# Performance work log

Hardware: AMD Instinct MI355X
Metric: run time of the kernel (lower is better)

Reference implementation:

```python
import jax, jax.numpy as jnp
import numpy as np

SDIM, VDIM, HID, DEPTH = 128, 3, 64, 4
N, E = 50000, 800000
CUTOFF = 5.0


def setup_inputs() -> dict:
    key = jax.random.key(0)
    ks = jax.random.split(key, 16)
    s = jax.random.normal(ks[0], (N, SDIM), jnp.float32)
    v = jax.random.normal(ks[1], (N, 3, VDIM), jnp.float32)
    edge_index = jax.random.randint(ks[2], (2, E), 0, N, dtype=jnp.int32).astype(jnp.int64)
    d = jax.random.uniform(ks[3], (E,), jnp.float32) * CUTOFF
    r = jax.random.normal(ks[4], (E, 3), jnp.float32)
    r = r / jnp.linalg.norm(r, axis=-1, keepdims=True)
    batch = jnp.zeros((N,), jnp.int64)

    def w(k, shape):
        return jax.random.normal(k, shape, jnp.float32) / jnp.sqrt(jnp.float32(shape[-2]))

    return {
        's': s, 'v': v, 'edge_index': edge_index, 'd': d, 'r': r, 'batch': batch,
        'We1': w(ks[5], (DEPTH, 2 * SDIM + 1, HID)), 'be1': jnp.zeros((DEPTH, HID), jnp.float32),
        'We2': w(ks[6], (DEPTH, HID, HID)), 'be2': jnp.zeros((DEPTH, HID), jnp.float32),
        'Wn1': w(ks[7], (DEPTH, SDIM + HID, HID)), 'bn1': jnp.zeros((DEPTH, HID), jnp.float32),
        'Wn2': w(ks[8], (DEPTH, HID, SDIM)), 'bn2': jnp.zeros((DEPTH, SDIM), jnp.float32),
        'Wv': w(ks[9], (DEPTH, HID, 2 * VDIM)), 'bv': jnp.zeros((DEPTH, 2 * VDIM), jnp.float32),
    }


def _egcl(s, v, src, dst, d, r, C, deg, We1, be1, We2, be2, Wn1, bn1, Wn2, bn2, Wv, bv):
    n = s.shape[0]
    # edge message MLP on gathered endpoint features + distance
    x = jnp.concatenate([s[dst], s[src], d[:, None]], axis=-1)   # [E, 2*SDIM+1]
    h = jax.nn.silu(x @ We1 + be1)
    h = jax.nn.silu(h @ We2 + be2)
    h = h * C[:, None]                                            # cutoff envelope
    # scalar update
    agg_s = jax.ops.segment_sum(h, dst, num_segments=n)           # [N, HID]
    u = jax.nn.silu(jnp.concatenate([s, agg_s], axis=-1) @ Wn1 + bn1)
    s = s + (u @ Wn2 + bn2)
    # equivariant vector update: gated neighbor vectors + gated edge directions
    gates = h @ Wv + bv                                           # [E, 2*VDIM]
    g1, g2 = gates[:, :VDIM], gates[:, VDIM:]
    mv = v[src] * g1[:, None, :] + r[:, :, None] * g2[:, None, :] # [E, 3, VDIM]
    agg_v = jax.ops.segment_sum(mv, dst, num_segments=n) / deg[:, None, None]  # mean aggr
    v = v + agg_v
    return s, v


def reference(s, v, edge_index, d, r, batch, We1, be1, We2, be2, Wn1, bn1, Wn2, bn2, Wv, bv):
    src, dst = edge_index[0], edge_index[1]
    C = 0.5 * (jnp.cos(jnp.pi * d / CUTOFF) + 1.0) * (d < CUTOFF).astype(d.dtype)
    deg = jax.ops.segment_sum(jnp.ones_like(d), dst, num_segments=s.shape[0])
    deg = jnp.maximum(deg, 1.0)
    for i in range(DEPTH):
        s, v = _egcl(s, v, src, dst, d, r, C, deg,
                     We1[i], be1[i], We2[i], be2[i],
                     Wn1[i], bn1[i], Wn2[i], bn2[i], Wv[i], bv[i])
    return (s, v)
```

## Files before the change

### kernel.cpp

```cpp
#include <hip/hip_runtime.h>
#include <math.h>

#define SDIM 128
#define HID 64
#define DEPTH 4
#define CUTOFF_F 5.0f
#define CHUNK 4096

typedef __attribute__((ext_vector_type(8))) short bf16x8;
typedef __attribute__((ext_vector_type(4))) float f32x4;
typedef float4 __attribute__((aligned(4))) float4_u;

__device__ __forceinline__ float silu_f(float x) {
    float e = __expf(-x);
    return x * __builtin_amdgcn_rcpf(1.0f + e);
}

__device__ __forceinline__ unsigned short f2bf(float x) {
    unsigned int u = __float_as_uint(x);
    unsigned int r = (u + 0x7fffu + ((u >> 16) & 1u)) >> 16;
    return (unsigned short)r;
}
__device__ __forceinline__ float bf2f(unsigned short u) {
    return __uint_as_float(((unsigned int)u) << 16);
}

struct f8 { float v[8]; };
__device__ __forceinline__ f8 load8(const float* p) {
    f8 r;
    float4 a = *(const float4*)p;
    float4 b = *(const float4*)(p + 4);
    r.v[0]=a.x; r.v[1]=a.y; r.v[2]=a.z; r.v[3]=a.w;
    r.v[4]=b.x; r.v[5]=b.y; r.v[6]=b.z; r.v[7]=b.w;
    return r;
}
__device__ __forceinline__ bf16x8 pack8(const float* h) {
    bf16x8 o;
#pragma unroll
    for (int j = 0; j < 8; ++j) o[j] = (short)f2bf(h[j]);
    return o;
}
__device__ __forceinline__ void unpack8(bf16x8 b, float* o) {
#pragma unroll
    for (int j = 0; j < 8; ++j)
        o[j] = __uint_as_float(((unsigned int)(unsigned short)b[j]) << 16);
}

__global__ void detect_idx_kernel(const void* ei, int N, int* flag) {
    int lane = threadIdx.x;
    const long long* p64 = (const long long*)ei;
    long long v = p64[lane];
    bool ok = (v >= 0 && v < (long long)N);
    unsigned long long m = __ballot(ok);
    if (lane == 0) *flag = (m == ~0ull) ? 1 : 0;
}

__global__ void decode_idx_kernel(const void* ei, int E, int N, const int* flag,
                                  int* __restrict__ srcw, int* __restrict__ dstw,
                                  int* __restrict__ deg_i) {
    int i = blockIdx.x * blockDim.x + threadIdx.x;
    if (i >= 2 * E) return;
    int v;
    if (*flag) v = (int)((const long long*)ei)[i];
    else       v = ((const int*)ei)[i];
    v = min(max(v, 0), N - 1);
    if (i < E) {
        srcw[i] = v;
    } else {
        dstw[i - E] = v;
        atomicAdd(&deg_i[v], 1);
    }
}

__global__ __launch_bounds__(256) void scan1_kernel(const int* __restrict__ deg_i,
                                                    int* __restrict__ part, int N) {
    __shared__ int wsum[4];
    int b = blockIdx.x, t = threadIdx.x;
    int base = b * CHUNK;
    int sum = 0;
    for (int i = t; i < CHUNK; i += 256) {
        int idx = base + i;
        sum += (idx < N) ? deg_i[idx] : 0;
    }
#pragma unroll
    for (int off = 32; off; off >>= 1) sum += __shfl_down(sum, off, 64);
    if ((t & 63) == 0) wsum[t >> 6] = sum;
    __syncthreads();
    if (t == 0) part[b] = wsum[0] + wsum[1] + wsum[2] + wsum[3];
}

__global__ void scan2_kernel(int* __restrict__ part, int* __restrict__ row_start,
                             int B1, int N) {
    int t = threadIdx.x;
    int v = (t < B1) ? part[t] : 0;
    int incl = v;
#pragma unroll
    for (int off = 1; off < 64; off <<= 1) {
        int x = __shfl_up(incl, off, 64);
        if (t >= off) incl += x;
    }
    if (t < B1) part[t] = incl - v;
    if (t == 63) row_start[N] = incl;
}

__global__ __launch_bounds__(256) void scan3_kernel(const int* __restrict__ deg_i,
                                                    const int* __restrict__ part,
                                                    int* __restrict__ row_start, int N) {
    __shared__ int wsum[4];
    __shared__ int carry_s;
    int b = blockIdx.x, t = threadIdx.x;
    int lane = t & 63, w = t >> 6;
    if (t == 0) carry_s = part[b];
    __syncthreads();
    int base0 = b * CHUNK;
    for (int base = base0; base < base0 + CHUNK; base += 256) {
        int i = base + t;
        int v = (i < N) ? deg_i[i] : 0;
        int incl = v;
#pragma unroll
        for (int off = 1; off < 64; off <<= 1) {
            int x = __shfl_up(incl, off, 64);
            if (lane >= off) incl += x;
        }
        if (lane == 63) wsum[w] = incl;
        __syncthreads();
        int wpre = 0;
#pragma unroll
        for (int k = 0; k < 4; ++k) if (k < w) wpre += wsum[k];
        int total = wsum[0] + wsum[1] + wsum[2] + wsum[3];
        int carry = carry_s;
        if (i < N) row_start[i] = carry + wpre + incl - v;
        __syncthreads();
        if (t == 0) carry_s = carry + total;
        __syncthreads();
    }
}

__global__ void scatter_kernel(const int* __restrict__ srcw, const int* __restrict__ dstw,
                               const float* __restrict__ dvec, const float* __restrict__ rvec,
                               const int* __restrict__ row_start, int* __restrict__ cursor,
                               float* __restrict__ rec, int E) {
    int e = blockIdx.x * blockDim.x + threadIdx.x;
    if (e >= E) return;
    int dd = dstw[e];
    int ofs = atomicAdd(&cursor[dd], 1);
    int pos = row_start[dd] + ofs;
    float dv = dvec[e];
    float c = 0.5f * (cosf(3.14159265358979323846f * dv * (1.0f / CUTOFF_F)) + 1.0f);
    c = (dv < CUTOFF_F) ? c : 0.0f;
    float4 r0 = make_float4(__int_as_float(srcw[e]), __int_as_float(dd), dv, c);
    float4 r1 = make_float4(rvec[(size_t)e * 3 + 0], rvec[(size_t)e * 3 + 1],
                            rvec[(size_t)e * 3 + 2], 0.0f);
    *(float4*)(rec + (size_t)pos * 8)     = r0;
    *(float4*)(rec + (size_t)pos * 8 + 4) = r1;
}

__global__ __launch_bounds__(256) void wprep_kernel(
    const float* __restrict__ We1, const float* __restrict__ We2,
    const float* __restrict__ Wv,  const float* __restrict__ Wn1,
    const float* __restrict__ Wn2,
    unsigned short* __restrict__ We1t, unsigned short* __restrict__ We2t,
    unsigned short* __restrict__ Wvt,  unsigned short* __restrict__ Wn1t,
    unsigned short* __restrict__ Wn2t) {
    int l = blockIdx.x, t = threadIdx.x;
    const float* W2 = We2 + (size_t)l * HID * HID;
    unsigned short* T2 = We2t + (size_t)l * HID * HID;
    for (int idx = t; idx < HID * HID; idx += 256) {
        int n = idx >> 6, k = idx & 63;
        T2[n * 64 + k] = f2bf(W2[k * HID + n]);
    }
    const float* Wvl = Wv + (size_t)l * HID * 6;
    unsigned short* Tv = Wvt + (size_t)l * 16 * 64;
    for (int idx = t; idx < 16 * 64; idx += 256) {
        int n = idx >> 6, k = idx & 63;
        Tv[idx] = (n < 6) ? f2bf(Wvl[k * 6 + n]) : (unsigned short)0;
    }
    const float* W1 = We1 + (size_t)l * 257 * 64;
    unsigned short* T1 = We1t + (size_t)l * 128 * 128;
    for (int idx = t; idx < 128 * 128; idx += 256) {
        int n = idx >> 7, k = idx & 127;
        float w = (n < 64) ? W1[(size_t)k * 64 + n] : W1[(size_t)(k + 128) * 64 + (n - 64)];
        T1[n * 128 + k] = f2bf(w);
    }
    const float* Wn1l = Wn1 + (size_t)l * 192 * 64;
    unsigned short* Tn1 = Wn1t + (size_t)l * 64 * 192;
    for (int idx = t; idx < 64 * 192; idx += 256) {
        int n = idx / 192, k = idx - n * 192;
        Tn1[idx] = f2bf(Wn1l[(size_t)k * 64 + n]);
    }
    const float* Wn2l = Wn2 + (size_t)l * 64 * 128;
    unsigned short* Tn2 = Wn2t + (size_t)l * 128 * 64;
    for (int idx = t; idx < 128 * 64; idx += 256) {
        int n = idx >> 6, k = idx & 63;
        Tn2[idx] = f2bf(Wn2l[(size_t)k * 128 + n]);
    }
}

__global__ __launch_bounds__(256) void node_pre_kernel(
    const float* __restrict__ s, const unsigned short* __restrict__ We1t,
    const float* __restrict__ be1,
    unsigned short* __restrict__ Pa, unsigned short* __restrict__ Pb, int N)
{
    __shared__ unsigned short sa[64 * 136];
    int t = threadIdx.x;
    int n0 = blockIdx.x * 64;
    for (int idx = t; idx < 64 * 32; idx += 256) {
        int rn = idx >> 5, c4 = (idx & 31) << 2;
        int n = n0 + rn;
        float4 val = make_float4(0.f, 0.f, 0.f, 0.f);
        if (n < N) val = *(const float4*)(s + (size_t)n * SDIM + c4);
        unsigned int p0 = (unsigned int)f2bf(val.x) | ((unsigned int)f2bf(val.y) << 16);
        unsigned int p1 = (unsigned int)f2bf(val.z) | ((unsigned int)f2bf(val.w) << 16);
        *(uint2*)(sa + rn * 136 + c4) = make_uint2(p0, p1);
    }
    __syncthreads();
    int lane = t & 63, w = t >> 6;
    int lm = lane & 15, lq = lane >> 4;
    int m0 = w * 16, rm = m0 + lm;

    bf16x8 af[4];
#pragma unroll
    for (int kc = 0; kc < 4; ++kc)
        af[kc] = *(const bf16x8*)(sa + rm * 136 + kc * 32 + lq * 8);

#pragma unroll
    for (int ct = 0; ct < 8; ++ct) {
        int col = ct * 16 + lm;
        f32x4 acc = {0.f, 0.f, 0.f, 0.f};
#pragma unroll
        for (int kc = 0; kc < 4; ++kc) {
            bf16x8 b = *(const bf16x8*)(We1t + (size_t)col * 128 + kc * 32 + lq * 8);
            acc = __builtin_amdgcn_mfma_f32_16x16x32_bf16(af[kc], b, acc, 0, 0, 0);
        }
        float bias = (ct < 4) ? be1[col] : 0.0f;
#pragma unroll
        for (int g = 0; g < 4; ++g) {
            int n = n0 + m0 + lq * 4 + g;
            if (n < N) {
                if (ct < 4) Pa[(size_t)n * HID + col]        = f2bf(acc[g] + bias);
                else        Pb[(size_t)n * HID + (col - 64)] = f2bf(acc[g]);
            }
        }
    }
}

__global__ __launch_bounds__(256) void edge_kernel(
    const float* __restrict__ rec,
    const unsigned short* __restrict__ Pa, const unsigned short* __restrict__ Pb,
    const float* __restrict__ wd,
    const unsigned short* __restrict__ We2t, const float* __restrict__ be2,
    const unsigned short* __restrict__ Wvt, const float* __restrict__ bv,
    const float* __restrict__ v,
    float* __restrict__ agg_s, float* __restrict__ agg_v, int E)
{
    __shared__ unsigned short hb[64 * 72];
    __shared__ float gl[64 * 8];
    __shared__ float vb[64 * 12];
    __shared__ int   m_src[64], m_dst[64];
    __shared__ float m_d[64], m_C[64];
    __shared__ float m_r[64 * 3];
    int t = threadIdx.x;
    int e0 = blockIdx.x * 64;
    if (t < 64) {
        int e = e0 + t;
        int ec = (e < E) ? e : (E - 1);
        float4 r0 = *(const float4*)(rec + (size_t)ec * 8);
        float4 r1 = *(const float4*)(rec + (size_t)ec * 8 + 4);
        m_src[t] = __float_as_int(r0.x);
        m_dst[t] = __float_as_int(r0.y);
        m_d[t]   = r0.z;
        m_C[t]   = (e < E) ? r0.w : 0.0f;
        m_r[t*3+0] = r1.x; m_r[t*3+1] = r1.y; m_r[t*3+2] = r1.z;
    }
    __syncthreads();

    int lane = t & 63;
    int w    = t >> 6;
    int lm = lane & 15, lq = lane >> 4;
    int m0 = w * 16;
    int rm = m0 + lm;
    int ka = lq * 8;
    int kb = 32 + lq * 8;

    if (t < 64) {
        const float* vr = v + (size_t)m_src[t] * 9;
        float4_u a = *(const float4_u*)vr;
        float4_u b = *(const float4_u*)(vr + 4);
        float c = vr[8];
        vb[t*12+0]=a.x; vb[t*12+1]=a.y; vb[t*12+2]=a.z; vb[t*12+3]=a.w;
        vb[t*12+4]=b.x; vb[t*12+5]=b.y; vb[t*12+6]=b.z; vb[t*12+7]=b.w;
        vb[t*12+8]=c;
    }
    bf16x8 wv0 = *(const bf16x8*)(Wvt + (size_t)lm * 64 + ka);
    bf16x8 wv1 = *(const bf16x8*)(Wvt + (size_t)lm * 64 + kb);

    bf16x8 afr0, afr1;
    {
        int dstr = m_dst[rm], srcr = m_src[rm];
        float dv = m_d[rm];
        const unsigned short* pa = Pa + (size_t)dstr * HID;
        const unsigned short* pb = Pb + (size_t)srcr * HID;
        bf16x8 ba0 = *(const bf16x8*)(pa + ka);
        bf16x8 bb0 = *(const bf16x8*)(pb + ka);
        bf16x8 ba1 = *(const bf16x8*)(pa + kb);
        bf16x8 bb1 = *(const bf16x8*)(pb + kb);
        f8 xw = load8(wd + ka), yw = load8(wd + kb);
        float fa[8], fb[8], h1[8];
        unpack8(ba0, fa); unpack8(bb0, fb);
#pragma unroll
        for (int j = 0; j < 8; ++j) h1[j] = silu_f(fa[j] + fb[j] + dv * xw.v[j]);
        afr0 = pack8(h1);
        unpack8(ba1, fa); unpack8(bb1, fb);
#pragma unroll
        for (int j = 0; j < 8; ++j) h1[j] = silu_f(fa[j] + fb[j] + dv * yw.v[j]);
        afr1 = pack8(h1);
    }

#pragma unroll
    for (int t4 = 0; t4 < 4; ++t4) {
        int col = t4 * 16 + lm;
        bf16x8 b0 = *(const bf16x8*)(We2t + (size_t)col * 64 + ka);
        bf16x8 b1 = *(const bf16x8*)(We2t + (size_t)col * 64 + kb);
        f32x4 a = {0.f, 0.f, 0.f, 0.f};
        a = __builtin_amdgcn_mfma_f32_16x16x32_bf16(afr0, b0, a, 0, 0, 0);
        a = __builtin_amdgcn_mfma_f32_16x16x32_bf16(afr1, b1, a, 0, 0, 0);
        float bias = be2[col];
#pragma unroll
        for (int g = 0; g < 4; ++g) {
            int er = m0 + lq * 4 + g;
            hb[er * 72 + col] = f2bf(silu_f(a[g] + bias) * m_C[er]);
        }
    }
    __syncthreads();

    {
        bf16x8 ga0 = *(const bf16x8*)(hb + rm * 72 + ka);
        bf16x8 ga1 = *(const bf16x8*)(hb + rm * 72 + kb);
        f32x4 ga = {0.f, 0.f, 0.f, 0.f};
        ga = __builtin_amdgcn_mfma_f32_16x16x32_bf16(ga0, wv0, ga, 0, 0, 0);
        ga = __builtin_amdgcn_mfma_f32_16x16x32_bf16(ga1, wv1, ga, 0, 0, 0);
        if (lm < 6) {
            float bias = bv[lm];
#pragma unroll
            for (int g = 0; g < 4; ++g) {
                int er = m0 + lq * 4 + g;
                gl[er * 8 + lm] = ga[g] + bias;
            }
        }
    }

    {
        int c = t & 63, seg = t >> 6;
        int r0 = seg * 16;
        float acc = 0.f;
        int cur = m_dst[r0];
#pragma unroll 4
        for (int r = r0; r < r0 + 16; ++r) {
            int dr = m_dst[r];
            if (dr != cur) {
                atomicAdd(&agg_s[(size_t)cur * HID + c], acc);
                acc = 0.f; cur = dr;
            }
            acc += bf2f(hb[r * 72 + c]);
        }
        atomicAdd(&agg_s[(size_t)cur * HID + c], acc);
    }
    __syncthreads();

    if (t < 144) {
        int seg = t / 9;
        int c = t - seg * 9;
        int i = c / 3, j = c - i * 3;
        int r0 = seg * 4;
        float acc = 0.f;
        int cur = m_dst[r0];
#pragma unroll
        for (int r = 0; r < 4; ++r) {
            int rr = r0 + r;
            int dr = m_dst[rr];
            if (dr != cur) {
                atomicAdd(&agg_v[(size_t)cur * 9 + c], acc);
                acc = 0.f; cur = dr;
            }
            if (e0 + rr < E) {
                acc += vb[rr * 12 + c] * gl[rr * 8 + j]
                     + m_r[rr * 3 + i] * gl[rr * 8 + 3 + j];
            }
        }
        atomicAdd(&agg_v[(size_t)cur * 9 + c], acc);
    }
}

__global__ __launch_bounds__(256) void node_fused_kernel(
    float* __restrict__ s, float* __restrict__ vout,
    float* __restrict__ agg_s, float* __restrict__ agg_v,
    const int* __restrict__ row_start,
    const unsigned short* __restrict__ Wn1t, const float* __restrict__ bn1,
    const unsigned short* __restrict__ Wn2t, const float* __restrict__ bn2,
    const unsigned short* __restrict__ We1tn, const float* __restrict__ be1n,
    unsigned short* __restrict__ Pa, unsigned short* __restrict__ Pb,
    int N, int do_pre)
{
    __shared__ unsigned short xa[64 * 200];
    __shared__ unsigned short ub[64 * 72];
    int t = threadIdx.x;
    int n0 = blockIdx.x * 64;
    for (int idx = t; idx < 64 * 32; idx += 256) {
        int rn = idx >> 5, c4 = (idx & 31) << 2;
        int n = n0 + rn;
        float4 val = make_float4(0.f, 0.f, 0.f, 0.f);
        if (n < N) val = *(const float4*)(s + (size_t)n * SDIM + c4);
        unsigned int p0 = (unsigned int)f2bf(val.x) | ((unsigned int)f2bf(val.y) << 16);
        unsigned int p1 = (unsigned int)f2bf(val.z) | ((unsigned int)f2bf(val.w) << 16);
        *(uint2*)(xa + rn * 200 + c4) = make_uint2(p0, p1);
    }
    for (int idx = t; idx < 64 * 16; idx += 256) {
        int rn = idx >> 4, c4 = (idx & 15) << 2;
        int n = n0 + rn;
        float4 val = make_float4(0.f, 0.f, 0.f, 0.f);
        if (n < N) {
            float* ap = agg_s + (size_t)n * HID + c4;
            val = *(const float4*)ap;
            *(float4*)ap = make_float4(0.f, 0.f, 0.f, 0.f);
        }
        unsigned int p0 = (unsigned int)f2bf(val.x) | ((unsigned int)f2bf(val.y) << 16);
        unsigned int p1 = (unsigned int)f2bf(val.z) | ((unsigned int)f2bf(val.w) << 16);
        *(uint2*)(xa + rn * 200 + 128 + c4) = make_uint2(p0, p1);
    }
    __syncthreads();

    int lane = t & 63, w = t >> 6;
    int lm = lane & 15, lq = lane >> 4;
    int m0 = w * 16, rm = m0 + lm;

    bf16x8 af[6];
#pragma unroll
    for (int kc = 0; kc < 6; ++kc)
        af[kc] = *(const bf16x8*)(xa + rm * 200 + kc * 32 + lq * 8);

#pragma unroll
    for (int ct = 0; ct < 4; ++ct) {
        int col = ct * 16 + lm;
        f32x4 acc = {0.f, 0.f, 0.f, 0.f};
#pragma unroll
        for (int kc = 0; kc < 6; ++kc) {
            bf16x8 b = *(const bf16x8*)(Wn1t + (size_t)col * 192 + kc * 32 + lq * 8);
            acc = __builtin_amdgcn_mfma_f32_16x16x32_bf16(af[kc], b, acc, 0, 0, 0);
        }
        float bias = bn1[col];
#pragma unroll
        for (int g = 0; g < 4; ++g) {
            int er = m0 + lq * 4 + g;
            ub[er * 72 + col] = f2bf(silu_f(acc[g] + bias));
        }
    }
    __syncthreads();

    unsigned short* sa = xa;
    bf16x8 uf[2];
#pragma unroll
    for (int kc = 0; kc < 2; ++kc)
        uf[kc] = *(const bf16x8*)(ub + rm * 72 + kc * 32 + lq * 8);

#pragma unroll
    for (int ct = 0; ct < 8; ++ct) {
        int col = ct * 16 + lm;
        f32x4 acc = {0.f, 0.f, 0.f, 0.f};
#pragma unroll
        for (int kc = 0; kc < 2; ++kc) {
            bf16x8 b = *(const bf16x8*)(Wn2t + (size_t)col * 64 + kc * 32 + lq * 8);
            acc = __builtin_amdgcn_mfma_f32_16x16x32_bf16(uf[kc], b, acc, 0, 0, 0);
        }
        float bias = bn2[col];
#pragma unroll
        for (int g = 0; g < 4; ++g) {
            int er = m0 + lq * 4 + g;
            int n = n0 + er;
            if (n < N) {
                float* sp = s + (size_t)n * SDIM + col;
                float sv = *sp + acc[g] + bias;
                *sp = sv;
                sa[er * 136 + col] = f2bf(sv);
            } else {
                sa[er * 136 + col] = 0;
            }
        }
    }
    __syncthreads();

    if (do_pre) {
        bf16x8 pf[4];
#pragma unroll
        for (int kc = 0; kc < 4; ++kc)
            pf[kc] = *(const bf16x8*)(sa + rm * 136 + kc * 32 + lq * 8);

#pragma unroll
        for (int ct = 0; ct < 8; ++ct) {
            int col = ct * 16 + lm;
            f32x4 acc = {0.f, 0.f, 0.f, 0.f};
#pragma unroll
            for (int kc = 0; kc < 4; ++kc) {
                bf16x8 b = *(const bf16x8*)(We1tn + (size_t)col * 128 + kc * 32 + lq * 8);
                acc = __builtin_amdgcn_mfma_f32_16x16x32_bf16(pf[kc], b, acc, 0, 0, 0);
            }
            float bias = (ct < 4) ? be1n[col] : 0.0f;
#pragma unroll
            for (int g = 0; g < 4; ++g) {
                int n = n0 + m0 + lq * 4 + g;
                if (n < N) {
                    if (ct < 4) Pa[(size_t)n * HID + col]        = f2bf(acc[g] + bias);
                    else        Pb[(size_t)n * HID + (col - 64)] = f2bf(acc[g]);
                }
            }
        }
    }

    for (int idx = t; idx < 64 * 9; idx += 256) {
        int rn = idx / 9, c = idx - rn * 9;
        int n2 = n0 + rn;
        if (n2 < N) {
            float av = agg_v[(size_t)n2 * 9 + c];
            agg_v[(size_t)n2 * 9 + c] = 0.f;
            float dg = fmaxf((float)(row_start[n2 + 1] - row_start[n2]), 1.0f);
            vout[(size_t)n2 * 9 + c] += av / dg;
        }
    }
}

extern "C" void kernel_launch(void* const* d_in, const int* in_sizes, int n_in,
                              void* d_out, int out_size, void* d_ws, size_t ws_size,
                              hipStream_t stream)
{
    const float* s_in  = (const float*)d_in[0];
    const float* v_in  = (const float*)d_in[1];
    const void*  ei    = d_in[2];
    const float* d_vec = (const float*)d_in[3];
    const float* r_vec = (const float*)d_in[4];
    const float* We1 = (const float*)d_in[6];
    const float* be1 = (const float*)d_in[7];
    const float* We2 = (const float*)d_in[8];
    const float* be2 = (const float*)d_in[9];
    const float* Wn1 = (const float*)d_in[10];
    const float* bn1 = (const float*)d_in[11];
    const float* Wn2 = (const float*)d_in[12];
    const float* bn2 = (const float*)d_in[13];
    const float* Wv  = (const float*)d_in[14];
    const float* bv  = (const float*)d_in[15];

    int N = in_sizes[0] / SDIM;
    int E = in_sizes[3];

    float* out_s = (float*)d_out;
    float* out_v = out_s + (size_t)N * SDIM;

    char* wp = (char*)d_ws;
    auto alloc = [&wp](size_t bytes) -> char* {
        char* p = wp;
        wp += (bytes + 31) & ~(size_t)31;
        return p;
    };
    float* rec       = (float*)alloc((size_t)E * 8 * 4);
    unsigned short* Pa = (unsigned short*)alloc((size_t)N * HID * 2);
    unsigned short* Pb = (unsigned short*)alloc((size_t)N * HID * 2);
    float* agg_s     = (float*)alloc((size_t)N * HID * 4);
    float* agg_v     = (float*)alloc((size_t)N * 9 * 4);
    int*   deg_i     = (int*)alloc((size_t)N * 4);
    int*   cursor    = (int*)alloc((size_t)N * 4);
    int*   row_start = (int*)alloc((size_t)(N + 1) * 4);
    int*   part      = (int*)alloc(64 * 4);
    int*   flag      = (int*)alloc(16);
    int*   srcw      = (int*)alloc((size_t)E * 4);
    int*   dstw      = (int*)alloc((size_t)E * 4);
    unsigned short* We2t = (unsigned short*)alloc((size_t)DEPTH * HID * HID * 2);
    unsigned short* Wvt  = (unsigned short*)alloc((size_t)DEPTH * 16 * 64 * 2);
    unsigned short* We1t = (unsigned short*)alloc((size_t)DEPTH * 128 * 128 * 2);
    unsigned short* Wn1t = (unsigned short*)alloc((size_t)DEPTH * 64 * 192 * 2);
    unsigned short* Wn2t = (unsigned short*)alloc((size_t)DEPTH * 128 * 64 * 2);

    hipMemcpyAsync(out_s, s_in, (size_t)N * SDIM * sizeof(float),
                   hipMemcpyDeviceToDevice, stream);
    hipMemcpyAsync(out_v, v_in, (size_t)N * 9 * sizeof(float),
                   hipMemcpyDeviceToDevice, stream);

    detect_idx_kernel<<<1, 64, 0, stream>>>(ei, N, flag);
    hipMemsetAsync(deg_i, 0, (size_t)N * 2 * sizeof(int), stream);
    hipMemsetAsync(agg_s, 0, (size_t)N * (HID + 9) * sizeof(float), stream);
    decode_idx_kernel<<<(2 * E + 255) / 256, 256, 0, stream>>>(ei, E, N, flag,
                                                               srcw, dstw, deg_i);
    int B1 = (N + CHUNK - 1) / CHUNK;
    scan1_kernel<<<B1, 256, 0, stream>>>(deg_i, part, N);
    scan2_kernel<<<1, 64, 0, stream>>>(part, row_start, B1, N);
    scan3_kernel<<<B1, 256, 0, stream>>>(deg_i, part, row_start, N);
    scatter_kernel<<<(E + 255) / 256, 256, 0, stream>>>(srcw, dstw, d_vec, r_vec,
                                                        row_start, cursor, rec, E);
    wprep_kernel<<<DEPTH, 256, 0, stream>>>(We1, We2, Wv, Wn1, Wn2,
                                            We1t, We2t, Wvt, Wn1t, Wn2t);

    int nb_n = (N + 63) / 64;
    int nb_e = (E + 63) / 64;
    node_pre_kernel<<<nb_n, 256, 0, stream>>>(out_s, We1t, be1, Pa, Pb, N);
    for (int l = 0; l < DEPTH; ++l) {
        int ln = (l + 1 < DEPTH) ? (l + 1) : 0;
        const float* We1_l = We1 + (size_t)l * 257 * 64;
        const float* be2_l = be2 + (size_t)l * 64;
        const float* bn1_l = bn1 + (size_t)l * 64;
        const float* bn2_l = bn2 + (size_t)l * 128;
        const float* bv_l  = bv  + (size_t)l * 6;
        const float* be1_n = be1 + (size_t)ln * 64;
        const unsigned short* We2t_l = We2t + (size_t)l * HID * HID;
        const unsigned short* Wvt_l  = Wvt  + (size_t)l * 16 * 64;
        const unsigned short* Wn1t_l = Wn1t + (size_t)l * 64 * 192;
        const unsigned short* Wn2t_l = Wn2t + (size_t)l * 128 * 64;
        const unsigned short* We1t_n = We1t + (size_t)ln * 128 * 128;

        edge_kernel<<<nb_e, 256, 0, stream>>>(rec, Pa, Pb,
                                              We1_l + 256 * 64,
                                              We2t_l, be2_l, Wvt_l, bv_l,
                                              out_v, agg_s, agg_v, E);
        node_fused_kernel<<<nb_n, 256, 0, stream>>>(out_s, out_v, agg_s, agg_v,
                                                    row_start,
                                                    Wn1t_l, bn1_l, Wn2t_l, bn2_l,
                                                    We1t_n, be1_n, Pa, Pb,
                                                    N, (l + 1 < DEPTH) ? 1 : 0);
    }
}
```

Baseline: 815.7 us.

## Stage edge records cooperatively in shared memory and use hardware bf16 conversion

The edge kernel now loads each block's 64 packed edge records with all 256 threads as coalesced float2 reads into one shared buffer, instead of 64 threads doing float4 loads into separate arrays. The v[src] gather is split across four threads per edge, and the cutoff factors are hoisted into registers. The gate MFMA operands are swapped so each lane holds one edge's gates, which allows a vectorized gate store. f2bf now uses the compiler's __bf16 conversion in place of manual rounding, which may lower to native conversion instructions and could treat NaNs differently.

```diff
diff --git a/kernel.cpp b/kernel.cpp
--- a/kernel.cpp
+++ b/kernel.cpp
@@ -17,9 +17,11 @@
 }
 
 __device__ __forceinline__ unsigned short f2bf(float x) {
-    unsigned int u = __float_as_uint(x);
-    unsigned int r = (u + 0x7fffu + ((u >> 16) & 1u)) >> 16;
-    return (unsigned short)r;
+    __bf16 b = (__bf16)x;
+    return __builtin_bit_cast(unsigned short, b);
+}
+__device__ __forceinline__ unsigned int f2bf2(float a, float b) {
+    return (unsigned int)f2bf(a) | ((unsigned int)f2bf(b) << 16);
 }
 __device__ __forceinline__ float bf2f(unsigned short u) {
     return __uint_as_float(((unsigned int)u) << 16);
@@ -209,9 +211,7 @@
         int n = n0 + rn;
         float4 val = make_float4(0.f, 0.f, 0.f, 0.f);
         if (n < N) val = *(const float4*)(s + (size_t)n * SDIM + c4);
-        unsigned int p0 = (unsigned int)f2bf(val.x) | ((unsigned int)f2bf(val.y) << 16);
-        unsigned int p1 = (unsigned int)f2bf(val.z) | ((unsigned int)f2bf(val.w) << 16);
-        *(uint2*)(sa + rn * 136 + c4) = make_uint2(p0, p1);
+        *(uint2*)(sa + rn * 136 + c4) = make_uint2(f2bf2(val.x, val.y), f2bf2(val.z, val.w));
     }
     __syncthreads();
     int lane = t & 63, w = t >> 6;
@@ -256,21 +256,22 @@
     __shared__ unsigned short hb[64 * 72];
     __shared__ float gl[64 * 8];
     __shared__ float vb[64 * 12];
-    __shared__ int   m_src[64], m_dst[64];
-    __shared__ float m_d[64], m_C[64];
-    __shared__ float m_r[64 * 3];
+    __shared__ float recb[64 * 8];
     int t = threadIdx.x;
     int e0 = blockIdx.x * 64;
-    if (t < 64) {
-        int e = e0 + t;
+
+    if (e0 + 64 <= E) {
+        float2 rv = *(const float2*)(rec + (size_t)e0 * 8 + 2 * t);
+        *(float2*)(recb + 2 * t) = rv;
+    } else {
+        int r = t >> 2, c = (t & 3) * 2;
+        int e = e0 + r;
         int ec = (e < E) ? e : (E - 1);
-        float4 r0 = *(const float4*)(rec + (size_t)ec * 8);
-        float4 r1 = *(const float4*)(rec + (size_t)ec * 8 + 4);
-        m_src[t] = __float_as_int(r0.x);
-        m_dst[t] = __float_as_int(r0.y);
-        m_d[t]   = r0.z;
-        m_C[t]   = (e < E) ? r0.w : 0.0f;
-        m_r[t*3+0] = r1.x; m_r[t*3+1] = r1.y; m_r[t*3+2] = r1.z;
+        float a  = rec[(size_t)ec * 8 + c];
+        float b2 = rec[(size_t)ec * 8 + c + 1];
+        if (e >= E && c == 2) b2 = 0.0f;
+        recb[2 * t]     = a;
+        recb[2 * t + 1] = b2;
     }
     __syncthreads();
 
@@ -282,22 +283,27 @@
     int ka = lq * 8;
     int kb = 32 + lq * 8;
 
-    if (t < 64) {
-        const float* vr = v + (size_t)m_src[t] * 9;
-        float4_u a = *(const float4_u*)vr;
-        float4_u b = *(const float4_u*)(vr + 4);
-        float c = vr[8];
-        vb[t*12+0]=a.x; vb[t*12+1]=a.y; vb[t*12+2]=a.z; vb[t*12+3]=a.w;
-        vb[t*12+4]=b.x; vb[t*12+5]=b.y; vb[t*12+6]=b.z; vb[t*12+7]=b.w;
-        vb[t*12+8]=c;
+    {
+        int r = t >> 2, p = t & 3;
+        const float* vr = v + (size_t)__float_as_int(recb[r * 8]) * 9;
+        if (p < 2) {
+            float4_u a = *(const float4_u*)(vr + p * 4);
+            vb[r * 12 + p * 4 + 0] = a.x;
+            vb[r * 12 + p * 4 + 1] = a.y;
+            vb[r * 12 + p * 4 + 2] = a.z;
+            vb[r * 12 + p * 4 + 3] = a.w;
+        } else if (p == 2) {
+            vb[r * 12 + 8] = vr[8];
+        }
     }
     bf16x8 wv0 = *(const bf16x8*)(Wvt + (size_t)lm * 64 + ka);
     bf16x8 wv1 = *(const bf16x8*)(Wvt + (size_t)lm * 64 + kb);
 
     bf16x8 afr0, afr1;
     {
-        int dstr = m_dst[rm], srcr = m_src[rm];
-        float dv = m_d[rm];
+        int srcr = __float_as_int(recb[rm * 8 + 0]);
+        int dstr = __float_as_int(recb[rm * 8 + 1]);
+        float dv = recb[rm * 8 + 2];
         const unsigned short* pa = Pa + (size_t)dstr * HID;
         const unsigned short* pb = Pb + (size_t)srcr * HID;
         bf16x8 ba0 = *(const bf16x8*)(pa + ka);
@@ -316,6 +322,9 @@
         afr1 = pack8(h1);
     }
 
+    float cc[4];
+#pragma unroll
+    for (int g = 0; g < 4; ++g) cc[g] = recb[(m0 + lq * 4 + g) * 8 + 3];
 #pragma unroll
     for (int t4 = 0; t4 < 4; ++t4) {
         int col = t4 * 16 + lm;
@@ -328,35 +337,36 @@
 #pragma unroll
         for (int g = 0; g < 4; ++g) {
             int er = m0 + lq * 4 + g;
-            hb[er * 72 + col] = f2bf(silu_f(a[g] + bias) * m_C[er]);
+            hb[er * 72 + col] = f2bf(silu_f(a[g] + bias) * cc[g]);
         }
     }
     __syncthreads();
 
     {
-        bf16x8 ga0 = *(const bf16x8*)(hb + rm * 72 + ka);
-        bf16x8 ga1 = *(const bf16x8*)(hb + rm * 72 + kb);
+        bf16x8 hb0 = *(const bf16x8*)(hb + rm * 72 + ka);
+        bf16x8 hb1 = *(const bf16x8*)(hb + rm * 72 + kb);
         f32x4 ga = {0.f, 0.f, 0.f, 0.f};
-        ga = __builtin_amdgcn_mfma_f32_16x16x32_bf16(ga0, wv0, ga, 0, 0, 0);
-        ga = __builtin_amdgcn_mfma_f32_16x16x32_bf16(ga1, wv1, ga, 0, 0, 0);
-        if (lm < 6) {
-            float bias = bv[lm];
-#pragma unroll
-            for (int g = 0; g < 4; ++g) {
-                int er = m0 + lq * 4 + g;
-                gl[er * 8 + lm] = ga[g] + bias;
-            }
+        ga = __builtin_amdgcn_mfma_f32_16x16x32_bf16(wv0, hb0, ga, 0, 0, 0);
+        ga = __builtin_amdgcn_mfma_f32_16x16x32_bf16(wv1, hb1, ga, 0, 0, 0);
+        int er2 = m0 + lm;
+        if (lq == 0) {
+            float4_u bb = *(const float4_u*)bv;
+            *(float4*)(gl + er2 * 8) =
+                make_float4(ga[0] + bb.x, ga[1] + bb.y, ga[2] + bb.z, ga[3] + bb.w);
+        } else if (lq == 1) {
+            gl[er2 * 8 + 4] = ga[0] + bv[4];
+            gl[er2 * 8 + 5] = ga[1] + bv[5];
         }
     }
 
     {
         int c = t & 63, seg = t >> 6;
-        int r0 = seg * 16;
+        int r0s = seg * 16;
         float acc = 0.f;
-        int cur = m_dst[r0];
+        int cur = __float_as_int(recb[r0s * 8 + 1]);
 #pragma unroll 4
-        for (int r = r0; r < r0 + 16; ++r) {
-            int dr = m_dst[r];
+        for (int r = r0s; r < r0s + 16; ++r) {
+            int dr = __float_as_int(recb[r * 8 + 1]);
             if (dr != cur) {
                 atomicAdd(&agg_s[(size_t)cur * HID + c], acc);
                 acc = 0.f; cur = dr;
@@ -371,20 +381,20 @@
         int seg = t / 9;
         int c = t - seg * 9;
         int i = c / 3, j = c - i * 3;
-        int r0 = seg * 4;
+        int r0v = seg * 4;
         float acc = 0.f;
-        int cur = m_dst[r0];
+        int cur = __float_as_int(recb[r0v * 8 + 1]);
 #pragma unroll
         for (int r = 0; r < 4; ++r) {
-            int rr = r0 + r;
-            int dr = m_dst[rr];
+            int rr = r0v + r;
+            int dr = __float_as_int(recb[rr * 8 + 1]);
             if (dr != cur) {
                 atomicAdd(&agg_v[(size_t)cur * 9 + c], acc);
                 acc = 0.f; cur = dr;
             }
             if (e0 + rr < E) {
                 acc += vb[rr * 12 + c] * gl[rr * 8 + j]
-                     + m_r[rr * 3 + i] * gl[rr * 8 + 3 + j];
+                     + recb[rr * 8 + 4 + i] * gl[rr * 8 + 3 + j];
             }
         }
         atomicAdd(&agg_v[(size_t)cur * 9 + c], acc);
@@ -410,9 +420,7 @@
         int n = n0 + rn;
         float4 val = make_float4(0.f, 0.f, 0.f, 0.f);
         if (n < N) val = *(const float4*)(s + (size_t)n * SDIM + c4);
-        unsigned int p0 = (unsigned int)f2bf(val.x) | ((unsigned int)f2bf(val.y) << 16);
-        unsigned int p1 = (unsigned int)f2bf(val.z) | ((unsigned int)f2bf(val.w) << 16);
-        *(uint2*)(xa + rn * 200 + c4) = make_uint2(p0, p1);
+        *(uint2*)(xa + rn * 200 + c4) = make_uint2(f2bf2(val.x, val.y), f2bf2(val.z, val.w));
     }
     for (int idx = t; idx < 64 * 16; idx += 256) {
         int rn = idx >> 4, c4 = (idx & 15) << 2;
@@ -423,9 +431,7 @@
             val = *(const float4*)ap;
             *(float4*)ap = make_float4(0.f, 0.f, 0.f, 0.f);
         }
-        unsigned int p0 = (unsigned int)f2bf(val.x) | ((unsigned int)f2bf(val.y) << 16);
-        unsigned int p1 = (unsigned int)f2bf(val.z) | ((unsigned int)f2bf(val.w) << 16);
-        *(uint2*)(xa + rn * 200 + 128 + c4) = make_uint2(p0, p1);
+        *(uint2*)(xa + rn * 200 + 128 + c4) = make_uint2(f2bf2(val.x, val.y), f2bf2(val.z, val.w));
     }
     __syncthreads();
 
```

Measured after the change: 823.1 us. Within noise of the previous version (+0.9%).
